# Optimization experiments

Measured on AMD Instinct MI355X. Metric: run time of the kernel, lower is better.

The kernel has to match this reference:

```python
import jax, jax.numpy as jnp
import numpy as np

N = 50000
E = 800000
D_IN = 256
D_H = 256


def setup_inputs() -> dict:
    key = jax.random.key(0)
    ks = jax.random.split(key, 8)
    x = jax.random.normal(ks[0], (N, D_IN), dtype=jnp.float32)
    W1 = jax.random.normal(ks[1], (D_H, D_IN), dtype=jnp.float32) * (1.0 / np.sqrt(D_IN))
    b1 = jnp.zeros((D_H,), dtype=jnp.float32)
    W2 = jax.random.normal(ks[2], (D_H, D_H), dtype=jnp.float32) * (1.0 / np.sqrt(D_H))
    b2 = jnp.zeros((D_H,), dtype=jnp.float32)
    gamma = jnp.ones((D_H,), dtype=jnp.float32)
    beta = jnp.zeros((D_H,), dtype=jnp.float32)
    adj_values = jax.random.uniform(ks[3], (E,), dtype=jnp.float32)
    rows = jax.random.randint(ks[4], (E,), 0, N, dtype=jnp.int64)
    cols = jax.random.randint(ks[5], (E,), 0, N, dtype=jnp.int64)
    adj_indices = jnp.stack([rows, cols], axis=0)
    return {"x": x, "W1": W1, "b1": b1, "W2": W2, "b2": b2,
            "gamma": gamma, "beta": beta, "adj_values": adj_values,
            "adj_indices": adj_indices}


def _spmm(adj_indices, adj_values, h, n):
    # out[i] = sum_j A[i, j] * h[j]; COO row=indices[0], col=indices[1]
    rows, cols = adj_indices[0], adj_indices[1]
    msgs = adj_values[:, None] * h[cols]          # [E, D]
    return jax.ops.segment_sum(msgs, rows, num_segments=n)


def _layernorm(h, gamma, beta, eps=1e-5):
    mu = jnp.mean(h, axis=-1, keepdims=True)
    var = jnp.var(h, axis=-1, keepdims=True)
    return (h - mu) * jax.lax.rsqrt(var + eps) * gamma + beta


def reference(x, W1, b1, W2, b2, gamma, beta, adj_values, adj_indices):
    n = x.shape[0]
    h = x @ W1.T + b1
    h = _spmm(adj_indices, adj_values, h, n)
    h = jax.nn.gelu(h, approximate=False)
    h = h @ W2.T + b2
    h = _spmm(adj_indices, adj_values, h, n)
    h = jax.nn.gelu(h, approximate=False)
    h = _layernorm(h + x[:, :h.shape[1]], gamma, beta)
    return h
```

## Files before the change

### kernel.cpp

```cpp
#include <hip/hip_runtime.h>
#include <math.h>

#define DH 256
#define CAP 64

typedef _Float16 f16x4 __attribute__((ext_vector_type(4)));
typedef _Float16 f16x8 __attribute__((ext_vector_type(8)));
typedef __fp16 fp16x2 __attribute__((ext_vector_type(2)));
typedef float f32x4 __attribute__((ext_vector_type(4)));

__device__ __forceinline__ float gelu_exact(float v) {
    return 0.5f * v * (1.0f + erff(v * 0.70710678118654752f));
}

__device__ __forceinline__ unsigned short f2h_bits(float f) {
    _Float16 h = (_Float16)f;
    return __builtin_bit_cast(unsigned short, h);
}

__device__ __forceinline__ _Float16 bits2h(unsigned short u) {
    return __builtin_bit_cast(_Float16, u);
}

__device__ __forceinline__ unsigned pk2h(float a, float b) {
    fp16x2 r = __builtin_amdgcn_cvt_pkrtz(a, b);
    return __builtin_bit_cast(unsigned, r);
}

__device__ __forceinline__ void async_copy16(const void* g, void* l) {
    __builtin_amdgcn_global_load_lds(
        (const __attribute__((address_space(1))) void*)g,
        (__attribute__((address_space(3))) void*)l, 16, 0, 0);
}

__global__ void prep_kernel(const float* __restrict__ W1, const float* __restrict__ W2,
                            unsigned short* __restrict__ W1h, unsigned short* __restrict__ W2h,
                            int* __restrict__ cnt, int n) {
    const int WV = DH * DH / 4;
    int gid = blockIdx.x * blockDim.x + threadIdx.x;
    if (gid < 2 * WV) {
        const float* src = (gid < WV) ? W1 : W2;
        unsigned short* dst = (gid < WV) ? W1h : W2h;
        int i = (gid < WV) ? gid : gid - WV;
        float4 v = *(const float4*)(src + (size_t)i * 4);
        uint2 o;
        o.x = pk2h(v.x, v.y);
        o.y = pk2h(v.z, v.w);
        *(uint2*)(dst + (size_t)i * 4) = o;
    } else {
        int i = (gid - 2 * WV) * 4;
        if (i < n) {
            int4 z = {0, 0, 0, 0};
            if (i + 4 <= n) *(int4*)(cnt + i) = z;
            else for (int k = i; k < n; ++k) cnt[k] = 0;
        }
    }
}

__global__ void bucket_kernel(const int* __restrict__ idx, const float* __restrict__ vals,
                              int* __restrict__ cnt, unsigned* __restrict__ cvb, int E) {
    int e = blockIdx.x * blockDim.x + threadIdx.x;
    if (e >= E) return;
    int r = idx[e];
    int c = idx[E + e];
    float v = vals[e];
    int p = atomicAdd(&cnt[r], 1);
    if (p < CAP) {
        cvb[(size_t)r * CAP + p] = ((unsigned)c << 16) | (unsigned)f2h_bits(v);
    }
}

template<bool AF32>
__global__ __launch_bounds__(512, 4) void gemm_mfma_kernel(
        const void* __restrict__ Ap, const unsigned short* __restrict__ Bh,
        const float* __restrict__ bias, unsigned short* __restrict__ C, int M) {
    __shared__ char smem[AF32 ? 65536 : 73728];
    char* bufB = smem;
    char* bufA = smem + 49152;
    const int tid  = threadIdx.x;
    const int lane = tid & 63;
    const int wid  = tid >> 6;
    const int m0   = blockIdx.x * 128;
    const int wm   = wid >> 2;
    const int wn   = wid & 3;
    const int l15  = lane & 15, l4 = lane >> 4;

    const int arow = tid >> 2;
    const int asw  = (tid & 3) ^ (arow & 3);
    int gra = m0 + arow; if (gra >= M) gra = M - 1;
    const float*     a32 = (const float*)Ap + (size_t)gra * DH + asw * 8;
    const _Float16*  a16 = (const _Float16*)Ap + (size_t)gra * DH + asw * 8;
    const unsigned short* b0p = Bh + (size_t)arow * DH + asw * 8;
    const unsigned short* b1p = Bh + (size_t)(arow + 128) * DH + asw * 8;

    float4 aLo[2], aHi[2];

    auto stageB = [&](int buf, int k0) {
        char* sB = bufB + buf * 16384;
        async_copy16(b0p + k0, sB + (size_t)(wid * 64) * 16);
        async_copy16(b1p + k0, sB + (size_t)(512 + wid * 64) * 16);
    };
    auto stageA16 = [&](int buf, int k0) {
        async_copy16(a16 + k0, bufA + buf * 8192 + (size_t)(wid * 64) * 16);
    };

    f32x4 acc[4][4] = {};

    if constexpr (AF32) {
        aLo[0] = *(const float4*)(a32 + 0);  aHi[0] = *(const float4*)(a32 + 4);
    } else {
        stageA16(0, 0);
    }
    stageB(0, 0);
    if constexpr (AF32) {
        aLo[1] = *(const float4*)(a32 + 32); aHi[1] = *(const float4*)(a32 + 36);
    } else {
        stageA16(1, 32);
    }
    stageB(1, 32);

    #pragma unroll
    for (int t = 0; t < 8; ++t) {
        if (t == 7)      { asm volatile("s_waitcnt vmcnt(0)" ::: "memory"); }
        else if (AF32)   { asm volatile("s_waitcnt vmcnt(4)" ::: "memory"); }
        else             { asm volatile("s_waitcnt vmcnt(3)" ::: "memory"); }
        if constexpr (AF32) {
            uint4 pk;
            pk.x = pk2h(aLo[t & 1].x, aLo[t & 1].y);
            pk.y = pk2h(aLo[t & 1].z, aLo[t & 1].w);
            pk.z = pk2h(aHi[t & 1].x, aHi[t & 1].y);
            pk.w = pk2h(aHi[t & 1].z, aHi[t & 1].w);
            *(uint4*)(bufA + (t & 1) * 8192 + (size_t)tid * 16) = pk;
            asm volatile("s_waitcnt lgkmcnt(0)" ::: "memory");
        }
        __builtin_amdgcn_s_barrier();
        __builtin_amdgcn_sched_barrier(0);

        char* sA = bufA + (AF32 ? (t & 1) : (t % 3)) * 8192;
        char* sB = bufB + (t % 3) * 16384;
        f16x8 af[4], bf[4];
        #pragma unroll
        for (int f = 0; f < 4; ++f) {
            int ra = wm * 64 + f * 16 + l15;
            int rb = wn * 64 + f * 16 + l15;
            int ca = (l4 ^ (ra & 3)) * 16;
            int cb = (l4 ^ (rb & 3)) * 16;
            af[f] = *(const f16x8*)(sA + ra * 64 + ca);
            bf[f] = *(const f16x8*)(sB + rb * 64 + cb);
        }
        #pragma unroll
        for (int fm = 0; fm < 4; ++fm)
            #pragma unroll
            for (int fn = 0; fn < 4; ++fn)
                acc[fm][fn] = __builtin_amdgcn_mfma_f32_16x16x32_f16(af[fm], bf[fn], acc[fm][fn], 0, 0, 0);

        if (t < 6) {
            int k0 = (t + 2) * 32;
            if constexpr (AF32) {
                aLo[t & 1] = *(const float4*)(a32 + k0);
                aHi[t & 1] = *(const float4*)(a32 + k0 + 4);
            } else {
                stageA16((t + 2) % 3, k0);
            }
            stageB((t + 2) % 3, k0);
        }
    }

    #pragma unroll
    for (int fn = 0; fn < 4; ++fn) {
        float bb = bias[wn * 64 + fn * 16 + l15];
        #pragma unroll
        for (int fm = 0; fm < 4; ++fm) {
            int mrow = m0 + wm * 64 + fm * 16 + l4 * 4;
            unsigned short* cp = C + (size_t)mrow * DH + wn * 64 + fn * 16 + l15;
            #pragma unroll
            for (int r = 0; r < 4; ++r) {
                if (mrow + r < M) cp[(size_t)r * DH] = f2h_bits(acc[fm][fn][r] + bb);
            }
        }
    }
}

template<int MODE>
__global__ __launch_bounds__(256) void spmm_kernel(
        const _Float16* __restrict__ h, const int* __restrict__ cnt,
        const unsigned* __restrict__ cvb, const float* __restrict__ xres,
        const float* __restrict__ gamma, const float* __restrict__ beta,
        void* __restrict__ outp, int n) {
    const int lane = threadIdx.x & 63;
    const int row = blockIdx.x * 4 + (threadIdx.x >> 6);
    if (row >= n) return;
    int deg = cnt[row]; if (deg > CAP) deg = CAP;
    const unsigned* cb = cvb + (size_t)row * CAP;

    f16x4 accA = {}, accB = {};
    int j = 0;
    for (; j + 4 <= deg; j += 4) {
        uint4 e = *(const uint4*)(cb + j);
        f16x4 p0 = *(const f16x4*)(h + (size_t)(e.x >> 16) * DH + lane * 4);
        f16x4 p1 = *(const f16x4*)(h + (size_t)(e.y >> 16) * DH + lane * 4);
        f16x4 p2 = *(const f16x4*)(h + (size_t)(e.z >> 16) * DH + lane * 4);
        f16x4 p3 = *(const f16x4*)(h + (size_t)(e.w >> 16) * DH + lane * 4);
        _Float16 v0 = bits2h((unsigned short)(e.x & 0xFFFFu));
        _Float16 v1 = bits2h((unsigned short)(e.y & 0xFFFFu));
        _Float16 v2 = bits2h((unsigned short)(e.z & 0xFFFFu));
        _Float16 v3 = bits2h((unsigned short)(e.w & 0xFFFFu));
        accA += p0 * v0; accB += p1 * v1;
        accA += p2 * v2; accB += p3 * v3;
    }
    for (; j < deg; ++j) {
        unsigned e = cb[j];
        f16x4 p0 = *(const f16x4*)(h + (size_t)(e >> 16) * DH + lane * 4);
        _Float16 v0 = bits2h((unsigned short)(e & 0xFFFFu));
        accA += p0 * v0;
    }

    float ax = (float)accA[0] + (float)accB[0];
    float ay = (float)accA[1] + (float)accB[1];
    float az = (float)accA[2] + (float)accB[2];
    float aw = (float)accA[3] + (float)accB[3];

    ax = gelu_exact(ax); ay = gelu_exact(ay); az = gelu_exact(az); aw = gelu_exact(aw);

    if (MODE == 1) {
        float4 xr = *(const float4*)(xres + (size_t)row * DH + lane * 4);
        ax += xr.x; ay += xr.y; az += xr.z; aw += xr.w;
        float s  = ax + ay + az + aw;
        float s2 = ax * ax + ay * ay + az * az + aw * aw;
        #pragma unroll
        for (int off = 32; off > 0; off >>= 1) {
            s  += __shfl_xor(s,  off);
            s2 += __shfl_xor(s2, off);
        }
        float mu  = s * (1.0f / 256.0f);
        float var = s2 * (1.0f / 256.0f) - mu * mu;
        float rs  = rsqrtf(var + 1e-5f);
        float4 g  = *(const float4*)(gamma + lane * 4);
        float4 bt = *(const float4*)(beta + lane * 4);
        float4 o;
        o.x = (ax - mu) * rs * g.x + bt.x;
        o.y = (ay - mu) * rs * g.y + bt.y;
        o.z = (az - mu) * rs * g.z + bt.z;
        o.w = (aw - mu) * rs * g.w + bt.w;
        *(float4*)((float*)outp + (size_t)row * DH + lane * 4) = o;
    } else {
        uint2 pk;
        pk.x = pk2h(ax, ay);
        pk.y = pk2h(az, aw);
        *(uint2*)((_Float16*)outp + (size_t)row * DH + lane * 4) = pk;
    }
}

extern "C" void kernel_launch(void* const* d_in, const int* in_sizes, int n_in,
                              void* d_out, int out_size, void* d_ws, size_t ws_size,
                              hipStream_t stream) {
    const float* x     = (const float*)d_in[0];
    const float* W1    = (const float*)d_in[1];
    const float* b1    = (const float*)d_in[2];
    const float* W2    = (const float*)d_in[3];
    const float* b2    = (const float*)d_in[4];
    const float* gamma = (const float*)d_in[5];
    const float* beta  = (const float*)d_in[6];
    const float* avals = (const float*)d_in[7];
    const int*   aidx  = (const int*)d_in[8];

    const int n = in_sizes[0] / DH;
    const int e = in_sizes[7];
    float* out = (float*)d_out;

    _Float16* g1h = (_Float16*)d_out;

    char* ws = (char*)d_ws;
    size_t off = 0;
    _Float16* hb = (_Float16*)(ws + off);              off += (size_t)n * DH * 2;
    off = (off + 255) & ~(size_t)255;
    unsigned short* W1h = (unsigned short*)(ws + off); off += (size_t)DH * DH * 2;
    off = (off + 255) & ~(size_t)255;
    unsigned short* W2h = (unsigned short*)(ws + off); off += (size_t)DH * DH * 2;
    off = (off + 255) & ~(size_t)255;
    int* cnt = (int*)(ws + off);                       off += (size_t)n * sizeof(int);
    off = (off + 255) & ~(size_t)255;
    unsigned* cvb = (unsigned*)(ws + off);             off += (size_t)n * CAP * sizeof(unsigned);

    const int gemm_gx = (n + 127) / 128;
    const int prep_items = 2 * (DH * DH / 4) + (n + 3) / 4;

    prep_kernel<<<(prep_items + 255) / 256, 256, 0, stream>>>(W1, W2, W1h, W2h, cnt, n);
    bucket_kernel<<<(e + 255) / 256, 256, 0, stream>>>(aidx, avals, cnt, cvb, e);

    gemm_mfma_kernel<true><<<gemm_gx, 512, 0, stream>>>(x, W1h, b1, (unsigned short*)hb, n);

    spmm_kernel<0><<<(n + 3) / 4, 256, 0, stream>>>(
        hb, cnt, cvb, nullptr, nullptr, nullptr, g1h, n);

    gemm_mfma_kernel<false><<<gemm_gx, 512, 0, stream>>>(g1h, W2h, b2, (unsigned short*)hb, n);

    spmm_kernel<1><<<(n + 3) / 4, 256, 0, stream>>>(
        hb, cnt, cvb, x, gamma, beta, out, n);
}
```

Baseline: 218.3 us.

## Store hidden features in column-sliced layout and gather per 32-wide slice in SpMM

The GEMM now writes its fp16 output as eight column slices of 32 features, each slice laid out [n][32], and the second GEMM reads its A operand from that sliced layout. SpMM is split into 8 blocks per row group, one per slice, with 8 edge groups per wave accumulating in fp32 and reducing via shuffles, so each gather touches a compact slice that is more likely to stay in L2/cache. LayerNorm moves into a separate kernel because a slice no longer sees the whole row, which adds an extra fp32 read and write of the output and more SpMM blocks.

```diff
diff --git a/kernel.cpp b/kernel.cpp
--- a/kernel.cpp
+++ b/kernel.cpp
@@ -88,8 +88,9 @@
     const int arow = tid >> 2;
     const int asw  = (tid & 3) ^ (arow & 3);
     int gra = m0 + arow; if (gra >= M) gra = M - 1;
-    const float*     a32 = (const float*)Ap + (size_t)gra * DH + asw * 8;
-    const _Float16*  a16 = (const _Float16*)Ap + (size_t)gra * DH + asw * 8;
+    const float*     a32  = (const float*)Ap + (size_t)gra * DH + asw * 8;
+    const _Float16*  a16s = (const _Float16*)Ap + (size_t)gra * 32 + asw * 8;
+    const size_t     aStep = (size_t)M * 32;
     const unsigned short* b0p = Bh + (size_t)arow * DH + asw * 8;
     const unsigned short* b1p = Bh + (size_t)(arow + 128) * DH + asw * 8;
 
@@ -100,8 +101,8 @@
         async_copy16(b0p + k0, sB + (size_t)(wid * 64) * 16);
         async_copy16(b1p + k0, sB + (size_t)(512 + wid * 64) * 16);
     };
-    auto stageA16 = [&](int buf, int k0) {
-        async_copy16(a16 + k0, bufA + buf * 8192 + (size_t)(wid * 64) * 16);
+    auto stageA16 = [&](int buf, int t) {
+        async_copy16(a16s + (size_t)t * aStep, bufA + buf * 8192 + (size_t)(wid * 64) * 16);
     };
 
     f32x4 acc[4][4] = {};
@@ -115,7 +116,7 @@
     if constexpr (AF32) {
         aLo[1] = *(const float4*)(a32 + 32); aHi[1] = *(const float4*)(a32 + 36);
     } else {
-        stageA16(1, 32);
+        stageA16(1, 1);
     }
     stageB(1, 32);
 
@@ -160,7 +161,7 @@
                 aLo[t & 1] = *(const float4*)(a32 + k0);
                 aHi[t & 1] = *(const float4*)(a32 + k0 + 4);
             } else {
-                stageA16((t + 2) % 3, k0);
+                stageA16((t + 2) % 3, t + 2);
             }
             stageB((t + 2) % 3, k0);
         }
@@ -168,87 +169,97 @@
 
     #pragma unroll
     for (int fn = 0; fn < 4; ++fn) {
-        float bb = bias[wn * 64 + fn * 16 + l15];
+        int col = wn * 64 + fn * 16 + l15;
+        float bb = bias[col];
+        unsigned short* base = C + ((size_t)(col >> 5) * M) * 32 + (col & 31);
         #pragma unroll
         for (int fm = 0; fm < 4; ++fm) {
             int mrow = m0 + wm * 64 + fm * 16 + l4 * 4;
-            unsigned short* cp = C + (size_t)mrow * DH + wn * 64 + fn * 16 + l15;
             #pragma unroll
             for (int r = 0; r < 4; ++r) {
-                if (mrow + r < M) cp[(size_t)r * DH] = f2h_bits(acc[fm][fn][r] + bb);
+                if (mrow + r < M) base[(size_t)(mrow + r) * 32] = f2h_bits(acc[fm][fn][r] + bb);
             }
         }
     }
 }
 
 template<int MODE>
-__global__ __launch_bounds__(256) void spmm_kernel(
-        const _Float16* __restrict__ h, const int* __restrict__ cnt,
+__global__ __launch_bounds__(256) void spmm_slice_kernel(
+        const _Float16* __restrict__ hs, const int* __restrict__ cnt,
         const unsigned* __restrict__ cvb, const float* __restrict__ xres,
-        const float* __restrict__ gamma, const float* __restrict__ beta,
         void* __restrict__ outp, int n) {
+    const int lane = threadIdx.x & 63;
+    const int wid  = threadIdx.x >> 6;
+    const int s    = blockIdx.x & 7;
+    const int row  = (blockIdx.x >> 3) * 4 + wid;
+    if (row >= n) return;
+    int deg = cnt[row]; if (deg > CAP) deg = CAP;
+    const unsigned* cb = cvb + (size_t)row * CAP;
+    const int eg = lane >> 3;
+    const int dl = lane & 7;
+    const _Float16* hss = hs + (size_t)s * n * 32 + dl * 4;
+
+    float a0 = 0.f, a1 = 0.f, a2 = 0.f, a3 = 0.f;
+    for (int j = eg; j < deg; j += 8) {
+        unsigned e = cb[j];
+        f16x4 p = *(const f16x4*)(hss + (size_t)(e >> 16) * 32);
+        float v = (float)bits2h((unsigned short)(e & 0xFFFFu));
+        a0 += v * (float)p[0];
+        a1 += v * (float)p[1];
+        a2 += v * (float)p[2];
+        a3 += v * (float)p[3];
+    }
+    #pragma unroll
+    for (int st = 8; st < 64; st <<= 1) {
+        a0 += __shfl_xor(a0, st);
+        a1 += __shfl_xor(a1, st);
+        a2 += __shfl_xor(a2, st);
+        a3 += __shfl_xor(a3, st);
+    }
+
+    if (lane < 8) {
+        a0 = gelu_exact(a0); a1 = gelu_exact(a1);
+        a2 = gelu_exact(a2); a3 = gelu_exact(a3);
+        if (MODE == 1) {
+            const float* xp = xres + (size_t)row * DH + s * 32 + dl * 4;
+            float4 xr = *(const float4*)xp;
+            float4 o = {a0 + xr.x, a1 + xr.y, a2 + xr.z, a3 + xr.w};
+            *(float4*)((float*)outp + (size_t)row * DH + s * 32 + dl * 4) = o;
+        } else {
+            uint2 pk;
+            pk.x = pk2h(a0, a1);
+            pk.y = pk2h(a2, a3);
+            *(uint2*)((_Float16*)outp + ((size_t)s * n + row) * 32 + dl * 4) = pk;
+        }
+    }
+}
+
+__global__ __launch_bounds__(256) void ln_kernel(
+        float* __restrict__ y, const float* __restrict__ gamma,
+        const float* __restrict__ beta, int n) {
     const int lane = threadIdx.x & 63;
     const int row = blockIdx.x * 4 + (threadIdx.x >> 6);
     if (row >= n) return;
-    int deg = cnt[row]; if (deg > CAP) deg = CAP;
-    const unsigned* cb = cvb + (size_t)row * CAP;
-
-    f16x4 accA = {}, accB = {};
-    int j = 0;
-    for (; j + 4 <= deg; j += 4) {
-        uint4 e = *(const uint4*)(cb + j);
-        f16x4 p0 = *(const f16x4*)(h + (size_t)(e.x >> 16) * DH + lane * 4);
-        f16x4 p1 = *(const f16x4*)(h + (size_t)(e.y >> 16) * DH + lane * 4);
-        f16x4 p2 = *(const f16x4*)(h + (size_t)(e.z >> 16) * DH + lane * 4);
-        f16x4 p3 = *(const f16x4*)(h + (size_t)(e.w >> 16) * DH + lane * 4);
-        _Float16 v0 = bits2h((unsigned short)(e.x & 0xFFFFu));
-        _Float16 v1 = bits2h((unsigned short)(e.y & 0xFFFFu));
-        _Float16 v2 = bits2h((unsigned short)(e.z & 0xFFFFu));
-        _Float16 v3 = bits2h((unsigned short)(e.w & 0xFFFFu));
-        accA += p0 * v0; accB += p1 * v1;
-        accA += p2 * v2; accB += p3 * v3;
-    }
-    for (; j < deg; ++j) {
-        unsigned e = cb[j];
-        f16x4 p0 = *(const f16x4*)(h + (size_t)(e >> 16) * DH + lane * 4);
-        _Float16 v0 = bits2h((unsigned short)(e & 0xFFFFu));
-        accA += p0 * v0;
-    }
-
-    float ax = (float)accA[0] + (float)accB[0];
-    float ay = (float)accA[1] + (float)accB[1];
-    float az = (float)accA[2] + (float)accB[2];
-    float aw = (float)accA[3] + (float)accB[3];
-
-    ax = gelu_exact(ax); ay = gelu_exact(ay); az = gelu_exact(az); aw = gelu_exact(aw);
-
-    if (MODE == 1) {
-        float4 xr = *(const float4*)(xres + (size_t)row * DH + lane * 4);
-        ax += xr.x; ay += xr.y; az += xr.z; aw += xr.w;
-        float s  = ax + ay + az + aw;
-        float s2 = ax * ax + ay * ay + az * az + aw * aw;
-        #pragma unroll
-        for (int off = 32; off > 0; off >>= 1) {
-            s  += __shfl_xor(s,  off);
-            s2 += __shfl_xor(s2, off);
-        }
-        float mu  = s * (1.0f / 256.0f);
-        float var = s2 * (1.0f / 256.0f) - mu * mu;
-        float rs  = rsqrtf(var + 1e-5f);
-        float4 g  = *(const float4*)(gamma + lane * 4);
-        float4 bt = *(const float4*)(beta + lane * 4);
-        float4 o;
-        o.x = (ax - mu) * rs * g.x + bt.x;
-        o.y = (ay - mu) * rs * g.y + bt.y;
-        o.z = (az - mu) * rs * g.z + bt.z;
-        o.w = (aw - mu) * rs * g.w + bt.w;
-        *(float4*)((float*)outp + (size_t)row * DH + lane * 4) = o;
-    } else {
-        uint2 pk;
-        pk.x = pk2h(ax, ay);
-        pk.y = pk2h(az, aw);
-        *(uint2*)((_Float16*)outp + (size_t)row * DH + lane * 4) = pk;
-    }
+    float* yp = y + (size_t)row * DH + lane * 4;
+    float4 v = *(const float4*)yp;
+    float sv  = v.x + v.y + v.z + v.w;
+    float sv2 = v.x * v.x + v.y * v.y + v.z * v.z + v.w * v.w;
+    #pragma unroll
+    for (int off = 32; off > 0; off >>= 1) {
+        sv  += __shfl_xor(sv,  off);
+        sv2 += __shfl_xor(sv2, off);
+    }
+    float mu  = sv * (1.0f / 256.0f);
+    float var = sv2 * (1.0f / 256.0f) - mu * mu;
+    float rs  = rsqrtf(var + 1e-5f);
+    float4 g  = *(const float4*)(gamma + lane * 4);
+    float4 bt = *(const float4*)(beta + lane * 4);
+    float4 o;
+    o.x = (v.x - mu) * rs * g.x + bt.x;
+    o.y = (v.y - mu) * rs * g.y + bt.y;
+    o.z = (v.z - mu) * rs * g.z + bt.z;
+    o.w = (v.w - mu) * rs * g.w + bt.w;
+    *(float4*)yp = o;
 }
 
 extern "C" void kernel_launch(void* const* d_in, const int* in_sizes, int n_in,
@@ -268,7 +279,7 @@
     const int e = in_sizes[7];
     float* out = (float*)d_out;
 
-    _Float16* g1h = (_Float16*)d_out;
+    _Float16* g1s = (_Float16*)d_out;
 
     char* ws = (char*)d_ws;
     size_t off = 0;
@@ -284,17 +295,18 @@
 
     const int gemm_gx = (n + 127) / 128;
     const int prep_items = 2 * (DH * DH / 4) + (n + 3) / 4;
+    const int spmm_grid = ((n + 3) / 4) * 8;
 
     prep_kernel<<<(prep_items + 255) / 256, 256, 0, stream>>>(W1, W2, W1h, W2h, cnt, n);
     bucket_kernel<<<(e + 255) / 256, 256, 0, stream>>>(aidx, avals, cnt, cvb, e);
 
     gemm_mfma_kernel<true><<<gemm_gx, 512, 0, stream>>>(x, W1h, b1, (unsigned short*)hb, n);
 
-    spmm_kernel<0><<<(n + 3) / 4, 256, 0, stream>>>(
-        hb, cnt, cvb, nullptr, nullptr, nullptr, g1h, n);
-
-    gemm_mfma_kernel<false><<<gemm_gx, 512, 0, stream>>>(g1h, W2h, b2, (unsigned short*)hb, n);
-
-    spmm_kernel<1><<<(n + 3) / 4, 256, 0, stream>>>(
-        hb, cnt, cvb, x, gamma, beta, out, n);
-}
+    spmm_slice_kernel<0><<<spmm_grid, 256, 0, stream>>>(hb, cnt, cvb, nullptr, g1s, n);
+
+    gemm_mfma_kernel<false><<<gemm_gx, 512, 0, stream>>>(g1s, W2h, b2, (unsigned short*)hb, n);
+
+    spmm_slice_kernel<1><<<spmm_grid, 256, 0, stream>>>(hb, cnt, cvb, x, out, n);
+
+    ln_kernel<<<(n + 3) / 4, 256, 0, stream>>>(out, gamma, beta, n);
+}
```

New measurement: 416.2 us. 1.91x slower.

## Merge GEMM1, edge bucketing and W2 conversion into one heterogeneous launch

Applied to the files above, without the earlier changes.

The first GEMM, the COO edge bucketing and the W2 fp16 conversion now run as block ranges of a single kernel launch, instead of as separate bucket, prep and GEMM kernels. W1 conversion and count zeroing stay in a smaller prep kernel. This removes one launch and lets the atomic-heavy bucketing run alongside the MFMA GEMM blocks. In exchange, the bucketing and conversion blocks now reserve the GEMM's 64KB of shared memory and 512-thread shape, which may limit how many of them fit per CU.

```diff
diff --git a/kernel.cpp b/kernel.cpp
--- a/kernel.cpp
+++ b/kernel.cpp
@@ -33,22 +33,19 @@
         (__attribute__((address_space(3))) void*)l, 16, 0, 0);
 }
 
-__global__ void prep_kernel(const float* __restrict__ W1, const float* __restrict__ W2,
-                            unsigned short* __restrict__ W1h, unsigned short* __restrict__ W2h,
+__global__ void prep_kernel(const float* __restrict__ W1,
+                            unsigned short* __restrict__ W1h,
                             int* __restrict__ cnt, int n) {
     const int WV = DH * DH / 4;
     int gid = blockIdx.x * blockDim.x + threadIdx.x;
-    if (gid < 2 * WV) {
-        const float* src = (gid < WV) ? W1 : W2;
-        unsigned short* dst = (gid < WV) ? W1h : W2h;
-        int i = (gid < WV) ? gid : gid - WV;
-        float4 v = *(const float4*)(src + (size_t)i * 4);
+    if (gid < WV) {
+        float4 v = *(const float4*)(W1 + (size_t)gid * 4);
         uint2 o;
         o.x = pk2h(v.x, v.y);
         o.y = pk2h(v.z, v.w);
-        *(uint2*)(dst + (size_t)i * 4) = o;
-    } else {
-        int i = (gid - 2 * WV) * 4;
+        *(uint2*)(W1h + (size_t)gid * 4) = o;
+    } else {
+        int i = (gid - WV) * 4;
         if (i < n) {
             int4 z = {0, 0, 0, 0};
             if (i + 4 <= n) *(int4*)(cnt + i) = z;
@@ -57,30 +54,16 @@
     }
 }
 
-__global__ void bucket_kernel(const int* __restrict__ idx, const float* __restrict__ vals,
-                              int* __restrict__ cnt, unsigned* __restrict__ cvb, int E) {
-    int e = blockIdx.x * blockDim.x + threadIdx.x;
-    if (e >= E) return;
-    int r = idx[e];
-    int c = idx[E + e];
-    float v = vals[e];
-    int p = atomicAdd(&cnt[r], 1);
-    if (p < CAP) {
-        cvb[(size_t)r * CAP + p] = ((unsigned)c << 16) | (unsigned)f2h_bits(v);
-    }
-}
-
 template<bool AF32>
-__global__ __launch_bounds__(512, 4) void gemm_mfma_kernel(
+__device__ __forceinline__ void gemm_body(char* smem,
         const void* __restrict__ Ap, const unsigned short* __restrict__ Bh,
-        const float* __restrict__ bias, unsigned short* __restrict__ C, int M) {
-    __shared__ char smem[AF32 ? 65536 : 73728];
+        const float* __restrict__ bias, unsigned short* __restrict__ C,
+        int M, int m0) {
     char* bufB = smem;
     char* bufA = smem + 49152;
     const int tid  = threadIdx.x;
     const int lane = tid & 63;
     const int wid  = tid >> 6;
-    const int m0   = blockIdx.x * 128;
     const int wm   = wid >> 2;
     const int wn   = wid & 3;
     const int l15  = lane & 15, l4 = lane >> 4;
@@ -179,6 +162,48 @@
             }
         }
     }
+}
+
+__global__ __launch_bounds__(512, 4) void phase1_kernel(
+        const float* __restrict__ x, const unsigned short* __restrict__ W1h,
+        const float* __restrict__ b1, unsigned short* __restrict__ hb, int M,
+        const int* __restrict__ aidx, const float* __restrict__ avals,
+        int* __restrict__ cnt, unsigned* __restrict__ cvb, int E,
+        const float* __restrict__ W2, unsigned short* __restrict__ W2h,
+        int GX, int BB) {
+    __shared__ char smem[65536];
+    const int bx = blockIdx.x;
+    if (bx < GX) {
+        gemm_body<true>(smem, x, W1h, b1, hb, M, bx * 128);
+    } else if (bx < GX + BB) {
+        int e = (bx - GX) * 512 + threadIdx.x;
+        if (e < E) {
+            int r = aidx[e];
+            int c = aidx[E + e];
+            float v = avals[e];
+            int p = atomicAdd(&cnt[r], 1);
+            if (p < CAP) {
+                cvb[(size_t)r * CAP + p] = ((unsigned)c << 16) | (unsigned)f2h_bits(v);
+            }
+        }
+    } else {
+        int i = (bx - GX - BB) * 512 + threadIdx.x;
+        if (i < DH * DH / 4) {
+            float4 v = *(const float4*)(W2 + (size_t)i * 4);
+            uint2 o;
+            o.x = pk2h(v.x, v.y);
+            o.y = pk2h(v.z, v.w);
+            *(uint2*)(W2h + (size_t)i * 4) = o;
+        }
+    }
+}
+
+template<bool AF32>
+__global__ __launch_bounds__(512, 4) void gemm_mfma_kernel(
+        const void* __restrict__ Ap, const unsigned short* __restrict__ Bh,
+        const float* __restrict__ bias, unsigned short* __restrict__ C, int M) {
+    __shared__ char smem[AF32 ? 65536 : 73728];
+    gemm_body<AF32>(smem, Ap, Bh, bias, C, M, blockIdx.x * 128);
 }
 
 template<int MODE>
@@ -283,12 +308,15 @@
     unsigned* cvb = (unsigned*)(ws + off);             off += (size_t)n * CAP * sizeof(unsigned);
 
     const int gemm_gx = (n + 127) / 128;
-    const int prep_items = 2 * (DH * DH / 4) + (n + 3) / 4;
-
-    prep_kernel<<<(prep_items + 255) / 256, 256, 0, stream>>>(W1, W2, W1h, W2h, cnt, n);
-    bucket_kernel<<<(e + 255) / 256, 256, 0, stream>>>(aidx, avals, cnt, cvb, e);
-
-    gemm_mfma_kernel<true><<<gemm_gx, 512, 0, stream>>>(x, W1h, b1, (unsigned short*)hb, n);
+    const int bucket_blks = (e + 511) / 512;
+    const int w2_blks = (DH * DH / 4 + 511) / 512;
+    const int prep_items = DH * DH / 4 + (n + 3) / 4;
+
+    prep_kernel<<<(prep_items + 255) / 256, 256, 0, stream>>>(W1, W1h, cnt, n);
+
+    phase1_kernel<<<gemm_gx + bucket_blks + w2_blks, 512, 0, stream>>>(
+        x, W1h, b1, (unsigned short*)hb, n,
+        aidx, avals, cnt, cvb, e, W2, W2h, gemm_gx, bucket_blks);
 
     spmm_kernel<0><<<(n + 3) / 4, 256, 0, stream>>>(
         hb, cnt, cvb, nullptr, nullptr, nullptr, g1h, n);
```

Result: no change. 219.7 us (+0.6%).
